# Kernel tuning notes

Measured on AMD Instinct MI355X. Metric: run time of the kernel, lower is better.

## Reference

```python
import jax, jax.numpy as jnp
import numpy as np

LAMBDA_COLOR = 10.0


def _neighbors(x, p):
    """Patch-unfold: x [B,C,H,W] -> [B, P*P, C, H, W] of zero-padded shifted copies.
    Matches conv3d with diagonal one-hot [P^2,1,1,P,P] weights, padding (0,pad,pad)."""
    pad = (p - 1) // 2
    B, C, H, W = x.shape
    xp = jnp.pad(x, ((0, 0), (0, 0), (pad, pad), (pad, pad)))
    shifts = [xp[:, :, i:i + H, j:j + W] for i in range(p) for j in range(p)]
    return jnp.stack(shifts, axis=1)


def _spatial_grid(img_size):
    # np.mgrid[-1:1+eps:2/(S-1), -1:1+eps:2/(S-1)] -> [2, S, S] (y-coords, x-coords)
    lin = jnp.linspace(-1.0, 1.0, img_size, dtype=jnp.float32)
    gy, gx = jnp.meshgrid(lin, lin, indexing='ij')
    return jnp.stack([gy, gx], axis=0)[None]  # [1, 2, S, S]


def setup_inputs() -> dict:
    key = jax.random.key(0)
    k1, k2 = jax.random.split(key)
    B, S, P = 16, 256, 7
    flow = jax.random.normal(k1, (B, 2, S, S), dtype=jnp.float32)
    image = jax.random.uniform(k2, (B, 3, S, S), dtype=jnp.float32)
    return {"flow": flow, "image": image, "img_size": S, "patch_size": P}


def reference(flow, image, img_size, patch_size):
    flow = flow * img_size                                  # [B,2,H,W]
    grid = _spatial_grid(img_size)                          # [1,2,H,W]

    flow_nb = _neighbors(flow, patch_size)                  # [B,P2,2,H,W]
    img_nb = _neighbors(image, patch_size)                  # [B,P2,3,H,W]
    grid_nb = _neighbors(grid, patch_size)                  # [1,P2,2,H,W]

    im_w = jnp.sum((image[:, None] - img_nb) ** 2, axis=2)  # [B,P2,H,W]
    sp_w = jnp.sum((grid[:, None] - grid_nb) ** 2, axis=2)  # [1,P2,H,W]
    fl = jnp.sum((flow_nb - flow[:, None]) ** 2, axis=2)    # [B,P2,H,W]

    return jnp.mean(fl * jnp.exp(-(im_w * LAMBDA_COLOR + sp_w)))
```

## Files before the change

### kernel.cpp

```cpp
#include <hip/hip_runtime.h>


#define S_DIM 256
#define LOG2E 1.4426950408889634f
#define C10L2E (-14.426950408889634f)
#define N_TERMS 51380224.0f
#define FINAL_SCALE (65536.0f / N_TERMS)

typedef float v4f __attribute__((ext_vector_type(4)));
typedef int   v4i __attribute__((ext_vector_type(4)));

__device__ v4f llvm_amdgcn_raw_buffer_load_v4f32(v4i rsrc, int voffset,
                                                 int soffset, int aux)
    __asm("llvm.amdgcn.raw.buffer.load.v4f32");

__device__ inline v4i make_srd(const void* p, unsigned bytes) {
    union { v4i v; unsigned u[4]; } s;
    s.u[0] = (unsigned)(unsigned long long)p;
    s.u[1] = (unsigned)(((unsigned long long)p) >> 32);
    s.u[2] = bytes;
    s.u[3] = 0x00020000u;
    return s.v;
}

__global__ __launch_bounds__(256, 2) void flow_reg_loss_kernel(
    const float* __restrict__ flow,
    const float* __restrict__ image,
    float* __restrict__ out)
{
    __shared__ float wave_sums[4];

    const int lane = threadIdx.x;
    const int wv   = threadIdx.y;
    const int y0   = (blockIdx.x * 4 + wv) * 2;
    const int b    = blockIdx.z;
    const int x0   = lane * 4;

    const v4i srdI = make_srd(image, 16u * 3u * 65536u * 4u);
    const v4i srdF = make_srd(flow,  16u * 2u * 65536u * 4u);

    const int rowx = x0 * 4 - 16;
    const int ib = b * 786432;
    const int fb = b * 524288;

    const float step = 2.0f / 255.0f;
    const float K2L2E = step * step * LOG2E;

#define LOAD_ROW(r, yy)                                                        \
    do {                                                                       \
        const int ro = (yy) * 1024 + rowx;                                     \
        _Pragma("unroll")                                                      \
        for (int c = 0; c < 3; ++c) {                                          \
            const int v = ib + c * 262144 + ro;                                \
            const v4f a  = llvm_amdgcn_raw_buffer_load_v4f32(srdI, v, 0, 0);   \
            const v4f b4 = llvm_amdgcn_raw_buffer_load_v4f32(srdI, v, 16, 0);  \
            const v4f c4 = llvm_amdgcn_raw_buffer_load_v4f32(srdI, v, 32, 0);  \
            r[c][0] = a.x;  r[c][1] = a.y;  r[c][2]  = a.z;  r[c][3]  = a.w;   \
            r[c][4] = b4.x; r[c][5] = b4.y; r[c][6]  = b4.z; r[c][7]  = b4.w;  \
            r[c][8] = c4.x; r[c][9] = c4.y; r[c][10] = c4.z; r[c][11] = c4.w;  \
        }                                                                      \
        _Pragma("unroll")                                                      \
        for (int c = 0; c < 2; ++c) {                                          \
            const int v = fb + c * 262144 + ro;                                \
            const v4f a  = llvm_amdgcn_raw_buffer_load_v4f32(srdF, v, 0, 0);   \
            const v4f b4 = llvm_amdgcn_raw_buffer_load_v4f32(srdF, v, 16, 0);  \
            const v4f c4 = llvm_amdgcn_raw_buffer_load_v4f32(srdF, v, 32, 0);  \
            r[3+c][0] = a.x;  r[3+c][1] = a.y;  r[3+c][2]  = a.z;              \
            r[3+c][3] = a.w;  r[3+c][4] = b4.x; r[3+c][5]  = b4.y;             \
            r[3+c][6] = b4.z; r[3+c][7] = b4.w; r[3+c][8]  = c4.x;             \
            r[3+c][9] = c4.y; r[3+c][10] = c4.z; r[3+c][11] = c4.w;            \
        }                                                                      \
    } while (0)

    float A[5][12], B[5][12];
    LOAD_ROW(A, y0);
    LOAD_ROW(B, y0 + 1);

    float wL[12];
#pragma unroll
    for (int j = 0; j < 12; ++j)
        wL[j] = ((unsigned)(x0 - 4 + j) < S_DIM) ? 1.0f : 0.0f;

    float ic0[2][4], ic1[2][4], ic2[2][4], fc0[2][4], fc1[2][4];
    float acc[4] = {0.f, 0.f, 0.f, 0.f};

    auto tap_row = [&](int cr, const float (&r)[5][12], int dy, int dx0) {
#pragma unroll
        for (int dx = dx0; dx <= 3; ++dx) {
            const float c2 = -K2L2E * (float)(dy * dy + dx * dx);
#pragma unroll
            for (int i = 0; i < 4; ++i) {
                const int j = i + dx + 4;
                const float d0 = ic0[cr][i] - r[0][j];
                const float d1 = ic1[cr][i] - r[1][j];
                const float d2 = ic2[cr][i] - r[2][j];
                const float imw = d0 * d0 + d1 * d1 + d2 * d2;
                const float e0 = r[3][j] - fc0[cr][i];
                const float e1 = r[4][j] - fc1[cr][i];
                const float fl2 = e0 * e0 + e1 * e1;
                acc[i] += (wL[j] * fl2) *
                          __builtin_amdgcn_exp2f(fmaf(imw, C10L2E, c2));
            }
        }
    };

#pragma unroll
    for (int i = 0; i < 4; ++i) {
        ic0[0][i] = A[0][4 + i]; ic1[0][i] = A[1][4 + i]; ic2[0][i] = A[2][4 + i];
        fc0[0][i] = A[3][4 + i]; fc1[0][i] = A[4][4 + i];
    }
    tap_row(0, A, 0, 1);
    LOAD_ROW(A, y0 + 2);

#pragma unroll
    for (int i = 0; i < 4; ++i) {
        ic0[1][i] = B[0][4 + i]; ic1[1][i] = B[1][4 + i]; ic2[1][i] = B[2][4 + i];
        fc0[1][i] = B[3][4 + i]; fc1[1][i] = B[4][4 + i];
    }
    tap_row(1, B, 0, 1);
    tap_row(0, B, 1, -3);
    LOAD_ROW(B, y0 + 3);

    if (y0 + 2 < S_DIM) {
        tap_row(0, A, 2, -3);
        tap_row(1, A, 1, -3);
    }
    LOAD_ROW(A, y0 + 4);

    if (y0 + 3 < S_DIM) {
        tap_row(0, B, 3, -3);
        tap_row(1, B, 2, -3);
    }

    if (y0 + 4 < S_DIM) {
        tap_row(1, A, 3, -3);
    }

    float oob = 0.0f;
#pragma unroll
    for (int cr = 0; cr < 2; ++cr) {
        const int yg = y0 + cr;
        const int ny_in = 7 - max(0, 3 - yg) - max(0, yg - (S_DIM - 1 - 3));
        const float gyc = -1.0f + step * (float)yg;
#pragma unroll
        for (int i = 0; i < 4; ++i) {
            const int xg = x0 + i;
            const int nx_in = 7 - max(0, 3 - xg) - max(0, xg - (S_DIM - 1 - 3));
            const float n_oob = (float)(49 - ny_in * nx_in);
            const float gxc = -1.0f + step * (float)xg;
            const float g2c = gyc * gyc + gxc * gxc;
            const float imw_c = ic0[cr][i] * ic0[cr][i] +
                                ic1[cr][i] * ic1[cr][i] +
                                ic2[cr][i] * ic2[cr][i];
            const float fl_c = fc0[cr][i] * fc0[cr][i] +
                               fc1[cr][i] * fc1[cr][i];
            oob += (n_oob * fl_c) *
                   __builtin_amdgcn_exp2f(fmaf(imw_c, C10L2E, -g2c * LOG2E));
        }
    }

    float acc_all = 2.0f * ((acc[0] + acc[1]) + (acc[2] + acc[3])) + oob;
#pragma unroll
    for (int off = 32; off > 0; off >>= 1)
        acc_all += __shfl_down(acc_all, off, 64);
    if (lane == 0) wave_sums[wv] = acc_all;
    __syncthreads();
    if (lane == 0 && wv == 0) {
        const float s =
            (wave_sums[0] + wave_sums[1]) + (wave_sums[2] + wave_sums[3]);
        atomicAdd(out, s * FINAL_SCALE);
    }
}

extern "C" void kernel_launch(void* const* d_in, const int* in_sizes, int n_in,
                              void* d_out, int out_size, void* d_ws, size_t ws_size,
                              hipStream_t stream) {
    const float* flow  = (const float*)d_in[0];
    const float* image = (const float*)d_in[1];
    float* out = (float*)d_out;

    dim3 grid(32, 1, 16);
    dim3 block(64, 4);
    flow_reg_loss_kernel<<<grid, block, 0, stream>>>(flow, image, out);
}
```

Baseline: 83.21 us.

## Process one center row per wave and fetch right halo via lane shuffles

Each wave now handles a single center row instead of two, doubling the grid, and loads only 8 floats per channel per row. The three right-halo columns are obtained from the neighbouring lane with __shfl_down instead of a third vector load. Launch bounds rise to 3 blocks per SIMD to raise occupancy. The cost is that each input row is loaded about twice as often, because reuse across paired center rows is lost, and shuffle instructions are added.

New measurement: 86.51 us. +4.0%, slower.

```diff
diff --git a/kernel.cpp b/kernel.cpp
--- a/kernel.cpp
+++ b/kernel.cpp
@@ -23,7 +23,7 @@
     return s.v;
 }
 
-__global__ __launch_bounds__(256, 2) void flow_reg_loss_kernel(
+__global__ __launch_bounds__(256, 3) void flow_reg_loss_kernel(
     const float* __restrict__ flow,
     const float* __restrict__ image,
     float* __restrict__ out)
@@ -32,7 +32,7 @@
 
     const int lane = threadIdx.x;
     const int wv   = threadIdx.y;
-    const int y0   = (blockIdx.x * 4 + wv) * 2;
+    const int y0   = blockIdx.x * 4 + wv;
     const int b    = blockIdx.z;
     const int x0   = lane * 4;
 
@@ -46,7 +46,7 @@
     const float step = 2.0f / 255.0f;
     const float K2L2E = step * step * LOG2E;
 
-#define LOAD_ROW(r, yy)                                                        \
+#define LOAD_ROW8(r, yy)                                                       \
     do {                                                                       \
         const int ro = (yy) * 1024 + rowx;                                     \
         _Pragma("unroll")                                                      \
@@ -54,49 +54,76 @@
             const int v = ib + c * 262144 + ro;                                \
             const v4f a  = llvm_amdgcn_raw_buffer_load_v4f32(srdI, v, 0, 0);   \
             const v4f b4 = llvm_amdgcn_raw_buffer_load_v4f32(srdI, v, 16, 0);  \
-            const v4f c4 = llvm_amdgcn_raw_buffer_load_v4f32(srdI, v, 32, 0);  \
-            r[c][0] = a.x;  r[c][1] = a.y;  r[c][2]  = a.z;  r[c][3]  = a.w;   \
-            r[c][4] = b4.x; r[c][5] = b4.y; r[c][6]  = b4.z; r[c][7]  = b4.w;  \
-            r[c][8] = c4.x; r[c][9] = c4.y; r[c][10] = c4.z; r[c][11] = c4.w;  \
+            r[c][0] = a.x;  r[c][1] = a.y;  r[c][2] = a.z;  r[c][3] = a.w;     \
+            r[c][4] = b4.x; r[c][5] = b4.y; r[c][6] = b4.z; r[c][7] = b4.w;    \
         }                                                                      \
         _Pragma("unroll")                                                      \
         for (int c = 0; c < 2; ++c) {                                          \
             const int v = fb + c * 262144 + ro;                                \
             const v4f a  = llvm_amdgcn_raw_buffer_load_v4f32(srdF, v, 0, 0);   \
             const v4f b4 = llvm_amdgcn_raw_buffer_load_v4f32(srdF, v, 16, 0);  \
-            const v4f c4 = llvm_amdgcn_raw_buffer_load_v4f32(srdF, v, 32, 0);  \
-            r[3+c][0] = a.x;  r[3+c][1] = a.y;  r[3+c][2]  = a.z;              \
-            r[3+c][3] = a.w;  r[3+c][4] = b4.x; r[3+c][5]  = b4.y;             \
-            r[3+c][6] = b4.z; r[3+c][7] = b4.w; r[3+c][8]  = c4.x;             \
-            r[3+c][9] = c4.y; r[3+c][10] = c4.z; r[3+c][11] = c4.w;            \
+            r[3+c][0] = a.x;  r[3+c][1] = a.y;  r[3+c][2] = a.z;               \
+            r[3+c][3] = a.w;  r[3+c][4] = b4.x; r[3+c][5] = b4.y;              \
+            r[3+c][6] = b4.z; r[3+c][7] = b4.w;                                \
         }                                                                      \
     } while (0)
 
-    float A[5][12], B[5][12];
-    LOAD_ROW(A, y0);
-    LOAD_ROW(B, y0 + 1);
+#define SHUF_ROW(s, r)                                                         \
+    do {                                                                       \
+        _Pragma("unroll")                                                      \
+        for (int c = 0; c < 5; ++c) {                                          \
+            s[c][0] = __shfl_down(r[c][4], 1, 64);                             \
+            s[c][1] = __shfl_down(r[c][5], 1, 64);                             \
+            s[c][2] = __shfl_down(r[c][6], 1, 64);                             \
+        }                                                                      \
+    } while (0)
 
-    float wL[12];
+    float A[5][8], B[5][8];
+    LOAD_ROW8(A, y0);
+    LOAD_ROW8(B, y0 + 1);
+
+    float wL[11];
 #pragma unroll
-    for (int j = 0; j < 12; ++j)
+    for (int j = 0; j < 11; ++j)
         wL[j] = ((unsigned)(x0 - 4 + j) < S_DIM) ? 1.0f : 0.0f;
 
-    float ic0[2][4], ic1[2][4], ic2[2][4], fc0[2][4], fc1[2][4];
+    float noob[4], g2l2e[4];
+    {
+        const int ny_in = 7 - max(0, 3 - y0) - max(0, y0 - (S_DIM - 1 - 3));
+        const float gyc = -1.0f + step * (float)y0;
+#pragma unroll
+        for (int i = 0; i < 4; ++i) {
+            const int xg = x0 + i;
+            const int nx_in = 7 - max(0, 3 - xg) - max(0, xg - (S_DIM - 1 - 3));
+            noob[i] = (float)(49 - ny_in * nx_in);
+            const float gxc = -1.0f + step * (float)xg;
+            g2l2e[i] = -(gyc * gyc + gxc * gxc) * LOG2E;
+        }
+    }
+
+    float ic0[4], ic1[4], ic2[4], fc0[4], fc1[4];
     float acc[4] = {0.f, 0.f, 0.f, 0.f};
 
-    auto tap_row = [&](int cr, const float (&r)[5][12], int dy, int dx0) {
+    float sA[5][3], sB[5][3];
+
+    auto tv = [](const float (&r)[8], const float (&s)[3], int j) -> float {
+        return (j < 8) ? r[j] : s[j - 8];
+    };
+
+    auto tap_row = [&](const float (&r)[5][8], const float (&s)[5][3],
+                       int dy, int dx0) {
 #pragma unroll
         for (int dx = dx0; dx <= 3; ++dx) {
             const float c2 = -K2L2E * (float)(dy * dy + dx * dx);
 #pragma unroll
             for (int i = 0; i < 4; ++i) {
                 const int j = i + dx + 4;
-                const float d0 = ic0[cr][i] - r[0][j];
-                const float d1 = ic1[cr][i] - r[1][j];
-                const float d2 = ic2[cr][i] - r[2][j];
+                const float d0 = ic0[i] - tv(r[0], s[0], j);
+                const float d1 = ic1[i] - tv(r[1], s[1], j);
+                const float d2 = ic2[i] - tv(r[2], s[2], j);
                 const float imw = d0 * d0 + d1 * d1 + d2 * d2;
-                const float e0 = r[3][j] - fc0[cr][i];
-                const float e1 = r[4][j] - fc1[cr][i];
+                const float e0 = tv(r[3], s[3], j) - fc0[i];
+                const float e1 = tv(r[4], s[4], j) - fc1[i];
                 const float fl2 = e0 * e0 + e1 * e1;
                 acc[i] += (wL[j] * fl2) *
                           __builtin_amdgcn_exp2f(fmaf(imw, C10L2E, c2));
@@ -106,57 +133,34 @@
 
 #pragma unroll
     for (int i = 0; i < 4; ++i) {
-        ic0[0][i] = A[0][4 + i]; ic1[0][i] = A[1][4 + i]; ic2[0][i] = A[2][4 + i];
-        fc0[0][i] = A[3][4 + i]; fc1[0][i] = A[4][4 + i];
+        ic0[i] = A[0][4 + i]; ic1[i] = A[1][4 + i]; ic2[i] = A[2][4 + i];
+        fc0[i] = A[3][4 + i]; fc1[i] = A[4][4 + i];
     }
-    tap_row(0, A, 0, 1);
-    LOAD_ROW(A, y0 + 2);
+    SHUF_ROW(sA, A);
+    tap_row(A, sA, 0, 1);
+    LOAD_ROW8(A, y0 + 2);
 
-#pragma unroll
-    for (int i = 0; i < 4; ++i) {
-        ic0[1][i] = B[0][4 + i]; ic1[1][i] = B[1][4 + i]; ic2[1][i] = B[2][4 + i];
-        fc0[1][i] = B[3][4 + i]; fc1[1][i] = B[4][4 + i];
-    }
-    tap_row(1, B, 0, 1);
-    tap_row(0, B, 1, -3);
-    LOAD_ROW(B, y0 + 3);
+    SHUF_ROW(sB, B);
+    tap_row(B, sB, 1, -3);
+    LOAD_ROW8(B, y0 + 3);
 
     if (y0 + 2 < S_DIM) {
-        tap_row(0, A, 2, -3);
-        tap_row(1, A, 1, -3);
+        SHUF_ROW(sA, A);
+        tap_row(A, sA, 2, -3);
     }
-    LOAD_ROW(A, y0 + 4);
 
     if (y0 + 3 < S_DIM) {
-        tap_row(0, B, 3, -3);
-        tap_row(1, B, 2, -3);
-    }
-
-    if (y0 + 4 < S_DIM) {
-        tap_row(1, A, 3, -3);
+        SHUF_ROW(sB, B);
+        tap_row(B, sB, 3, -3);
     }
 
     float oob = 0.0f;
 #pragma unroll
-    for (int cr = 0; cr < 2; ++cr) {
-        const int yg = y0 + cr;
-        const int ny_in = 7 - max(0, 3 - yg) - max(0, yg - (S_DIM - 1 - 3));
-        const float gyc = -1.0f + step * (float)yg;
-#pragma unroll
-        for (int i = 0; i < 4; ++i) {
-            const int xg = x0 + i;
-            const int nx_in = 7 - max(0, 3 - xg) - max(0, xg - (S_DIM - 1 - 3));
-            const float n_oob = (float)(49 - ny_in * nx_in);
-            const float gxc = -1.0f + step * (float)xg;
-            const float g2c = gyc * gyc + gxc * gxc;
-            const float imw_c = ic0[cr][i] * ic0[cr][i] +
-                                ic1[cr][i] * ic1[cr][i] +
-                                ic2[cr][i] * ic2[cr][i];
-            const float fl_c = fc0[cr][i] * fc0[cr][i] +
-                               fc1[cr][i] * fc1[cr][i];
-            oob += (n_oob * fl_c) *
-                   __builtin_amdgcn_exp2f(fmaf(imw_c, C10L2E, -g2c * LOG2E));
-        }
+    for (int i = 0; i < 4; ++i) {
+        const float imw_c = ic0[i] * ic0[i] + ic1[i] * ic1[i] + ic2[i] * ic2[i];
+        const float fl_c  = fc0[i] * fc0[i] + fc1[i] * fc1[i];
+        oob += (noob[i] * fl_c) *
+               __builtin_amdgcn_exp2f(fmaf(imw_c, C10L2E, g2l2e[i]));
     }
 
     float acc_all = 2.0f * ((acc[0] + acc[1]) + (acc[2] + acc[3])) + oob;
@@ -179,7 +183,7 @@
     const float* image = (const float*)d_in[1];
     float* out = (float*)d_out;
 
-    dim3 grid(32, 1, 16);
+    dim3 grid(64, 1, 16);
     dim3 block(64, 4);
     flow_reg_loss_kernel<<<grid, block, 0, stream>>>(flow, image, out);
 }
```
